# Performance work log

Hardware: AMD Instinct MI355X
Metric: run time of the kernel (lower is better)

The kernel has to match this reference:

```python
import jax, jax.numpy as jnp
import numpy as np

N = 8192
D_IN = 128
D_OUT = 128


def setup_inputs() -> dict:
    key = jax.random.key(0)
    k1, k2, k3 = jax.random.split(key, 3)
    node_features = jax.random.normal(k1, (N, D_IN), dtype=jnp.float32)
    adj_matrix = jax.random.uniform(k2, (N, N), dtype=jnp.float32)
    # Xavier-uniform weight, zero bias (as in reset_parameters)
    limit = float(np.sqrt(6.0 / (D_IN + D_OUT)))
    weight = jax.random.uniform(k3, (D_IN, D_OUT), dtype=jnp.float32,
                                minval=-limit, maxval=limit)
    bias = jnp.zeros((D_OUT,), dtype=jnp.float32)
    return {"node_features": node_features, "adj_matrix": adj_matrix,
            "weight": weight, "bias": bias}


def reference(node_features, adj_matrix, weight, bias):
    n = adj_matrix.shape[0]
    # A_hat = A + I
    a_hat = adj_matrix + jnp.eye(n, dtype=adj_matrix.dtype)
    d_hat = jnp.sum(a_hat, axis=1)  # [N]
    # pow(d, -0.5) with inf (d==0) masked to 0
    d_inv_sqrt = jnp.where(d_hat > 0, jax.lax.rsqrt(d_hat), 0.0)
    # diag(d) @ A_hat @ diag(d) == row/col broadcast scaling (same math)
    adj_normalized = d_inv_sqrt[:, None] * a_hat * d_inv_sqrt[None, :]
    support = node_features @ weight  # [N, D_OUT]
    out = adj_normalized @ support + bias
    return out
```

## Files before the change

kernel.cpp:

```cpp
#include <hip/hip_runtime.h>

#define NN 8192
#define DD 128

typedef short s16x4 __attribute__((ext_vector_type(4)));
typedef short s16x8 __attribute__((ext_vector_type(8)));
typedef float f32x4 __attribute__((ext_vector_type(4)));
typedef unsigned short u16;
typedef const void __attribute__((address_space(1))) gvoid;
typedef void __attribute__((address_space(3))) lvoid;

__device__ __forceinline__ u16 f2bf(float f) {
  unsigned int u = __float_as_uint(f);
  u += 0x7fffu + ((u >> 16) & 1u);
  return (u16)(u >> 16);
}
__device__ __forceinline__ float bf2f(u16 h) {
  return __uint_as_float(((unsigned int)h) << 16);
}

__global__ __launch_bounds__(256) void k_prep(const float* __restrict__ A,
                                              float* __restrict__ dinv,
                                              u16* __restrict__ Abf) {
  const int row = blockIdx.x;
  const float4* Ar = (const float4*)(A + (size_t)row * NN);
  ushort4* Br = (ushort4*)(Abf + (size_t)row * NN);
  const int t = threadIdx.x;
  float s = 0.f;
#pragma unroll
  for (int i = 0; i < 8; ++i) {
    float4 v = Ar[t + 256 * i];
    s += (v.x + v.y) + (v.z + v.w);
    ushort4 b;
    b.x = f2bf(v.x); b.y = f2bf(v.y); b.z = f2bf(v.z); b.w = f2bf(v.w);
    Br[t + 256 * i] = b;
  }
#pragma unroll
  for (int off = 32; off > 0; off >>= 1) s += __shfl_down(s, off, 64);
  __shared__ float red[4];
  if ((t & 63) == 0) red[t >> 6] = s;
  __syncthreads();
  if (t == 0) {
    float d = 1.0f + ((red[0] + red[1]) + (red[2] + red[3]));
    dinv[row] = d > 0.f ? rsqrtf(d) : 0.f;
  }
}

__global__ __launch_bounds__(256) void k_support(const float* __restrict__ X,
                                                 const float* __restrict__ W,
                                                 const float* __restrict__ dinv,
                                                 u16* __restrict__ tT) {
  __shared__ __align__(16) u16 Wt[128][136];
  __shared__ __align__(16) u16 Xs[32][136];
  const int t = threadIdx.x;
  const int j0 = blockIdx.x * 32;

  const float4* W4 = (const float4*)W;
#pragma unroll
  for (int s = 0; s < 16; ++s) {
    int c = t + 256 * s;
    int k = c >> 5, n4 = c & 31;
    float4 wv = W4[c];
    Wt[n4 * 4 + 0][k] = f2bf(wv.x);
    Wt[n4 * 4 + 1][k] = f2bf(wv.y);
    Wt[n4 * 4 + 2][k] = f2bf(wv.z);
    Wt[n4 * 4 + 3][k] = f2bf(wv.w);
  }
  const float4* X4 = (const float4*)(X + (size_t)j0 * DD);
#pragma unroll
  for (int s = 0; s < 4; ++s) {
    int c = t + 256 * s;
    int j = c >> 5, q = c & 31;
    float4 xv = X4[c];
    s16x4 p;
    p[0] = (short)f2bf(xv.x); p[1] = (short)f2bf(xv.y);
    p[2] = (short)f2bf(xv.z); p[3] = (short)f2bf(xv.w);
    *(s16x4*)&Xs[j][q * 4] = p;
  }
  __syncthreads();

  const int w = t >> 6, L = t & 63, lrow = L & 15, quad = L >> 4;
  f32x4 acc[2][2] = {};
#pragma unroll
  for (int ks = 0; ks < 4; ++ks) {
    const int k = ks * 32;
    s16x8 fa[2], fb[2];
#pragma unroll
    for (int nt = 0; nt < 2; ++nt)
      fa[nt] = *(const s16x8*)&Wt[w * 32 + nt * 16 + lrow][k + quad * 8];
#pragma unroll
    for (int jt = 0; jt < 2; ++jt)
      fb[jt] = *(const s16x8*)&Xs[jt * 16 + lrow][k + quad * 8];
#pragma unroll
    for (int nt = 0; nt < 2; ++nt)
#pragma unroll
      for (int jt = 0; jt < 2; ++jt)
        acc[nt][jt] = __builtin_amdgcn_mfma_f32_16x16x32_bf16(fa[nt], fb[jt], acc[nt][jt], 0, 0, 0);
  }

#pragma unroll
  for (int jt = 0; jt < 2; ++jt) {
    const int j = j0 + jt * 16 + lrow;
    const float dv = dinv[j];
#pragma unroll
    for (int nt = 0; nt < 2; ++nt) {
#pragma unroll
      for (int r = 0; r < 4; ++r) {
        const int n = w * 32 + nt * 16 + quad * 4 + r;
        tT[(size_t)n * NN + j] = f2bf(dv * acc[nt][jt][r]);
      }
    }
  }
}

__global__ __launch_bounds__(256, 2) void k_gemm(const u16* __restrict__ Abf,
                                                 const u16* __restrict__ tT,
                                                 float* __restrict__ part) {
  __shared__ __align__(16) unsigned char sh[2][32768];
  const int t = threadIdx.x;
  const int bm = blockIdx.x >> 3;
  const int kq = blockIdx.x & 7;
  const int kbase = kq * (NN / 8);
  const int w = t >> 6, L = t & 63, lrow = L & 15, quad = L >> 4;
  const int wr = w >> 1, wc = w & 1;
  const size_t row0 = (size_t)bm * 128;

  auto prefetch = [&](int buf, int k0) {
#pragma unroll
    for (int j = 0; j < 8; ++j) {
      const int g = w * 8 + j;
      const int o = g * 1024 + L * 16;
      const u16* src;
      if (g < 16) {
        const int r = o >> 7, c = (o >> 4) & 7;
        src = Abf + (row0 + r) * NN + (k0 + ((c ^ (r & 7)) << 3));
      } else {
        const int o2 = o - 16384;
        const int r = o2 >> 7, c = (o2 >> 4) & 7;
        src = tT + (size_t)r * NN + (k0 + ((c ^ (r & 7)) << 3));
      }
      __builtin_amdgcn_global_load_lds((gvoid*)src,
                                       (lvoid*)&sh[buf][g * 1024], 16, 0, 0);
    }
  };

  f32x4 acc[4][4] = {};
  prefetch(0, kbase);
  __syncthreads();

  for (int it = 0; it < 16; ++it) {
    const int cur = it & 1;
    if (it < 15) prefetch(cur ^ 1, kbase + (it + 1) * 64);
    const unsigned char* Ab = &sh[cur][0];
    const unsigned char* Bb = &sh[cur][16384];
#pragma unroll
    for (int s = 0; s < 2; ++s) {
      const int cx = (((s * 4) | quad) ^ (lrow & 7)) << 4;
      s16x8 fb[4];
#pragma unroll
      for (int nt = 0; nt < 4; ++nt)
        fb[nt] = *(const s16x8*)(Bb + (wc * 64 + nt * 16 + lrow) * 128 + cx);
#pragma unroll
      for (int mt = 0; mt < 4; ++mt) {
        s16x8 fa = *(const s16x8*)(Ab + (wr * 64 + mt * 16 + lrow) * 128 + cx);
#pragma unroll
        for (int nt = 0; nt < 4; ++nt)
          acc[mt][nt] = __builtin_amdgcn_mfma_f32_16x16x32_bf16(fa, fb[nt], acc[mt][nt], 0, 0, 0);
      }
    }
    __syncthreads();
  }

  float* pbase = part + (size_t)kq * NN * DD;
#pragma unroll
  for (int mt = 0; mt < 4; ++mt) {
#pragma unroll
    for (int r = 0; r < 4; ++r) {
      const int i = (int)row0 + wr * 64 + mt * 16 + quad * 4 + r;
#pragma unroll
      for (int nt = 0; nt < 4; ++nt) {
        const int n = wc * 64 + nt * 16 + lrow;
        pbase[(size_t)i * DD + n] = acc[mt][nt][r];
      }
    }
  }
}

__global__ __launch_bounds__(256) void k_reduce(const float* __restrict__ part,
                                                const u16* __restrict__ tT,
                                                const float* __restrict__ dinv,
                                                const float* __restrict__ bias,
                                                float* __restrict__ out) {
  const int gid = blockIdx.x * 256 + threadIdx.x;
  const int i = gid >> 5;
  const int c = gid & 31;
  const size_t idx = (size_t)i * 32 + c;
  float4 p[8];
#pragma unroll
  for (int q = 0; q < 8; ++q)
    p[q] = ((const float4*)(part + (size_t)q * NN * DD))[idx];
  float4 s;
  s.x = ((p[0].x + p[1].x) + (p[2].x + p[3].x)) + ((p[4].x + p[5].x) + (p[6].x + p[7].x));
  s.y = ((p[0].y + p[1].y) + (p[2].y + p[3].y)) + ((p[4].y + p[5].y) + (p[6].y + p[7].y));
  s.z = ((p[0].z + p[1].z) + (p[2].z + p[3].z)) + ((p[4].z + p[5].z) + (p[6].z + p[7].z));
  s.w = ((p[0].w + p[1].w) + (p[2].w + p[3].w)) + ((p[4].w + p[5].w) + (p[6].w + p[7].w));
  const float4 bb = ((const float4*)bias)[c];
  const float dv = dinv[i];
  const int n = c * 4;
  float4 o;
  o.x = dv * (s.x + bf2f(tT[(size_t)(n + 0) * NN + i])) + bb.x;
  o.y = dv * (s.y + bf2f(tT[(size_t)(n + 1) * NN + i])) + bb.y;
  o.z = dv * (s.z + bf2f(tT[(size_t)(n + 2) * NN + i])) + bb.z;
  o.w = dv * (s.w + bf2f(tT[(size_t)(n + 3) * NN + i])) + bb.w;
  ((float4*)out)[idx] = o;
}

extern "C" void kernel_launch(void* const* d_in, const int* in_sizes, int n_in,
                              void* d_out, int out_size, void* d_ws, size_t ws_size,
                              hipStream_t stream) {
  const float* X    = (const float*)d_in[0];
  const float* A    = (const float*)d_in[1];
  const float* W    = (const float*)d_in[2];
  const float* bias = (const float*)d_in[3];
  float* out = (float*)d_out;

  float* dinv = (float*)d_ws;
  u16*   tT   = (u16*)((char*)d_ws + 32768);
  float* part = (float*)((char*)d_ws + 32768 + 2097152);
  u16*   Abf  = (u16*)((char*)d_ws + 32768 + 2097152 + 33554432);

  hipLaunchKernelGGL(k_prep,    dim3(8192), dim3(256), 0, stream, A, dinv, Abf);
  hipLaunchKernelGGL(k_support, dim3(256),  dim3(256), 0, stream, X, W, dinv, tT);
  hipLaunchKernelGGL(k_gemm,    dim3(512),  dim3(256), 0, stream, Abf, tT, part);
  hipLaunchKernelGGL(k_reduce,  dim3(1024), dim3(256), 0, stream, part, tT, dinv, bias, out);
}
```

Measured before the change: 428.1 us.

## Fuse split-K reduction into GEMM epilogue via last-block atomic counter

Removes the separate reduce kernel. Each GEMM block now takes a ticket from a per-row-block atomic counter, and the last of the 8 split-K blocks sums the other partials and writes the final output with scaling, self-loop term and bias. A row-major copy of the scaled support matrix is added so the epilogue can read it coalesced, and the counters are zeroed in the prep kernel. This saves one launch and lets the reduction overlap with the remaining GEMM blocks, but it serialises the final sum onto one block per row tile and uses uncoalesced strided partial reads.

After: 560.2 us. 30.8% more time.

```diff
diff --git a/kernel.cpp b/kernel.cpp
--- a/kernel.cpp
+++ b/kernel.cpp
@@ -21,8 +21,10 @@
 
 __global__ __launch_bounds__(256) void k_prep(const float* __restrict__ A,
                                               float* __restrict__ dinv,
-                                              u16* __restrict__ Abf) {
+                                              u16* __restrict__ Abf,
+                                              unsigned int* __restrict__ cnt) {
   const int row = blockIdx.x;
+  if (row < 64 && threadIdx.x == 0) cnt[row] = 0u;
   const float4* Ar = (const float4*)(A + (size_t)row * NN);
   ushort4* Br = (ushort4*)(Abf + (size_t)row * NN);
   const int t = threadIdx.x;
@@ -49,7 +51,8 @@
 __global__ __launch_bounds__(256) void k_support(const float* __restrict__ X,
                                                  const float* __restrict__ W,
                                                  const float* __restrict__ dinv,
-                                                 u16* __restrict__ tT) {
+                                                 u16* __restrict__ tT,
+                                                 u16* __restrict__ tR) {
   __shared__ __align__(16) u16 Wt[128][136];
   __shared__ __align__(16) u16 Xs[32][136];
   const int t = threadIdx.x;
@@ -107,7 +110,9 @@
 #pragma unroll
       for (int r = 0; r < 4; ++r) {
         const int n = w * 32 + nt * 16 + quad * 4 + r;
-        tT[(size_t)n * NN + j] = f2bf(dv * acc[nt][jt][r]);
+        const u16 v = f2bf(dv * acc[nt][jt][r]);
+        tT[(size_t)n * NN + j] = v;
+        tR[(size_t)j * DD + n] = v;
       }
     }
   }
@@ -115,7 +120,12 @@
 
 __global__ __launch_bounds__(256, 2) void k_gemm(const u16* __restrict__ Abf,
                                                  const u16* __restrict__ tT,
-                                                 float* __restrict__ part) {
+                                                 const u16* __restrict__ tR,
+                                                 const float* __restrict__ dinv,
+                                                 const float* __restrict__ bias,
+                                                 float* __restrict__ part,
+                                                 unsigned int* __restrict__ cnt,
+                                                 float* __restrict__ out) {
   __shared__ __align__(16) unsigned char sh[2][32768];
   const int t = threadIdx.x;
   const int bm = blockIdx.x >> 3;
@@ -184,35 +194,39 @@
       }
     }
   }
-}
-
-__global__ __launch_bounds__(256) void k_reduce(const float* __restrict__ part,
-                                                const u16* __restrict__ tT,
-                                                const float* __restrict__ dinv,
-                                                const float* __restrict__ bias,
-                                                float* __restrict__ out) {
-  const int gid = blockIdx.x * 256 + threadIdx.x;
-  const int i = gid >> 5;
-  const int c = gid & 31;
-  const size_t idx = (size_t)i * 32 + c;
-  float4 p[8];
-#pragma unroll
-  for (int q = 0; q < 8; ++q)
-    p[q] = ((const float4*)(part + (size_t)q * NN * DD))[idx];
-  float4 s;
-  s.x = ((p[0].x + p[1].x) + (p[2].x + p[3].x)) + ((p[4].x + p[5].x) + (p[6].x + p[7].x));
-  s.y = ((p[0].y + p[1].y) + (p[2].y + p[3].y)) + ((p[4].y + p[5].y) + (p[6].y + p[7].y));
-  s.z = ((p[0].z + p[1].z) + (p[2].z + p[3].z)) + ((p[4].z + p[5].z) + (p[6].z + p[7].z));
-  s.w = ((p[0].w + p[1].w) + (p[2].w + p[3].w)) + ((p[4].w + p[5].w) + (p[6].w + p[7].w));
-  const float4 bb = ((const float4*)bias)[c];
-  const float dv = dinv[i];
-  const int n = c * 4;
-  float4 o;
-  o.x = dv * (s.x + bf2f(tT[(size_t)(n + 0) * NN + i])) + bb.x;
-  o.y = dv * (s.y + bf2f(tT[(size_t)(n + 1) * NN + i])) + bb.y;
-  o.z = dv * (s.z + bf2f(tT[(size_t)(n + 2) * NN + i])) + bb.z;
-  o.w = dv * (s.w + bf2f(tT[(size_t)(n + 3) * NN + i])) + bb.w;
-  ((float4*)out)[idx] = o;
+
+  __threadfence();
+  __shared__ unsigned int lastf;
+  if (t == 0) {
+    unsigned int prev = __hip_atomic_fetch_add(&cnt[bm], 1u, __ATOMIC_ACQ_REL,
+                                               __HIP_MEMORY_SCOPE_AGENT);
+    lastf = (prev == 7u) ? 1u : 0u;
+  }
+  __syncthreads();
+  if (lastf == 0u) return;
+  __threadfence();
+
+#pragma unroll
+  for (int mt = 0; mt < 4; ++mt) {
+#pragma unroll
+    for (int r = 0; r < 4; ++r) {
+      const int i = (int)row0 + wr * 64 + mt * 16 + quad * 4 + r;
+      const float dv = dinv[i];
+#pragma unroll
+      for (int nt = 0; nt < 4; ++nt) {
+        const int n = wc * 64 + nt * 16 + lrow;
+        const size_t off = (size_t)i * DD + n;
+        float q[8];
+#pragma unroll
+        for (int kk = 0; kk < 8; ++kk)
+          q[kk] = (kk == kq) ? acc[mt][nt][r]
+                             : part[(size_t)kk * NN * DD + off];
+        const float s = ((q[0] + q[1]) + (q[2] + q[3])) +
+                        ((q[4] + q[5]) + (q[6] + q[7]));
+        out[off] = dv * (s + bf2f(tR[off])) + bias[n];
+      }
+    }
+  }
 }
 
 extern "C" void kernel_launch(void* const* d_in, const int* in_sizes, int n_in,
@@ -224,13 +238,17 @@
   const float* bias = (const float*)d_in[3];
   float* out = (float*)d_out;
 
-  float* dinv = (float*)d_ws;
-  u16*   tT   = (u16*)((char*)d_ws + 32768);
-  float* part = (float*)((char*)d_ws + 32768 + 2097152);
-  u16*   Abf  = (u16*)((char*)d_ws + 32768 + 2097152 + 33554432);
-
-  hipLaunchKernelGGL(k_prep,    dim3(8192), dim3(256), 0, stream, A, dinv, Abf);
-  hipLaunchKernelGGL(k_support, dim3(256),  dim3(256), 0, stream, X, W, dinv, tT);
-  hipLaunchKernelGGL(k_gemm,    dim3(512),  dim3(256), 0, stream, Abf, tT, part);
-  hipLaunchKernelGGL(k_reduce,  dim3(1024), dim3(256), 0, stream, part, tT, dinv, bias, out);
-}
+  char* ws = (char*)d_ws;
+  float* dinv        = (float*)ws;
+  u16*   tT          = (u16*)(ws + 32768);
+  u16*   tR          = (u16*)(ws + 32768 + 2097152);
+  float* part        = (float*)(ws + 32768 + 2*2097152);
+  u16*   Abf         = (u16*)(ws + 32768 + 2*2097152 + 33554432);
+  unsigned int* cnt  = (unsigned int*)(ws + 32768 + 2*2097152 + 33554432
+                                          + 134217728);
+
+  hipLaunchKernelGGL(k_prep,    dim3(8192), dim3(256), 0, stream, A, dinv, Abf, cnt);
+  hipLaunchKernelGGL(k_support, dim3(256),  dim3(256), 0, stream, X, W, dinv, tT, tR);
+  hipLaunchKernelGGL(k_gemm,    dim3(512),  dim3(256), 0, stream,
+                     Abf, tT, tR, dinv, bias, part, cnt, out);
+}
```
